# Kernel tuning notes

Measured on AMD Instinct MI355X. Metric: run time of the kernel, lower is better.

## Reference

```python
import jax, jax.numpy as jnp
import numpy as np

N, D, E, K, CAP = 16384, 1024, 64, 2, 640

def setup_inputs() -> dict:
    key = jax.random.key(0)
    k1, k2, k3 = jax.random.split(key, 3)
    x = jax.random.normal(k1, (N, D), dtype=jnp.float32)
    Wr = jax.random.normal(k2, (D, E), dtype=jnp.float32) / np.sqrt(D)
    br = jnp.zeros((E,), dtype=jnp.float32)
    We = jax.random.normal(k3, (E, D, D), dtype=jnp.float32) / np.sqrt(D)
    return {"x": x, "Wr": Wr, "br": br, "We": We, "k": K, "capacity": CAP}

def _route(x, Wr, br, k, num_experts):
    logits = x @ Wr + br                                  # [N, E]
    top_k_vals, top_k_idxs = jax.lax.top_k(logits, k)     # [N, k]
    gates = jax.nn.softmax(top_k_vals, axis=-1)           # [N, k]
    # flatten k-major like the original: transpose((1,0)).flatten()
    flat = top_k_idxs.T.reshape(-1)                       # [k*N]
    expert_mask = (flat[:, None] == jnp.arange(num_experts)).astype(jnp.int32)
    buffer_idxs = jnp.cumsum(expert_mask, axis=0) * expert_mask - 1  # [k*N, E]
    buffer_idxs = buffer_idxs.reshape(k, -1, num_experts)            # [k, N, E]
    dispatch_idxs = buffer_idxs.transpose(2, 0, 1).max(axis=1)       # [E, N]
    combine_idxs = buffer_idxs.max(axis=-1).T                        # [N, k]
    return gates, top_k_idxs, dispatch_idxs, combine_idxs

def reference(x, Wr, br, We, k, capacity):
    num_experts = Wr.shape[1]
    gates, top_k_idxs, dispatch_idxs, combine_idxs = _route(x, Wr, br, k, num_experts)
    # dispatch: scatter tokens into per-expert capacity buffers; unassigned (-1)
    # and overflow (>= capacity) tokens land in the dropped slot `capacity`.
    d_idx = jnp.where((dispatch_idxs < 0) | (dispatch_idxs > capacity), capacity, dispatch_idxs)
    def scatter_one(idx):
        return jnp.zeros((capacity + 1, x.shape[-1]), x.dtype).at[idx].set(x)[:-1]
    dispatched = jax.vmap(scatter_one)(d_idx)             # [E, C, D]
    # per-expert linear (the wrap()/vmap-ed expert), grouped GEMM
    expert_out = jax.nn.relu(jnp.einsum('ecd,edh->ech', dispatched, We))
    # combine: gather back, pad row `capacity` yields zeros for dropped tokens
    padded = jnp.pad(expert_out, ((0, 0), (0, 1), (0, 0)))
    c_idx = jnp.where((combine_idxs < 0) | (combine_idxs > capacity), capacity, combine_idxs)
    combined = padded[top_k_idxs, c_idx]                  # [N, k, D]
    return jnp.einsum('nk,nkd->nd', gates, combined)      # [N, D]
```

## Files before the change

### kernel.cpp

```cpp
#include <hip/hip_runtime.h>
#include <hip/hip_bf16.h>
#include <cstdint>
#include <cstddef>

#define N_TOK 16384
#define DIM   1024
#define NEXP  64
#define CAPACITY 640

typedef __bf16 bf16x8 __attribute__((ext_vector_type(8)));
typedef float  f32x4  __attribute__((ext_vector_type(4)));

__device__ __forceinline__ unsigned short f2bf(float f) {
    union { float f; unsigned int u; } a; a.f = f;
    unsigned int r = a.u + 0x7FFFu + ((a.u >> 16) & 1u);
    return (unsigned short)(r >> 16);
}

__global__ __launch_bounds__(256) void router_convert(
    const float* __restrict__ x, const float* __restrict__ Wr,
    const float* __restrict__ br, const float* __restrict__ We,
    unsigned short* __restrict__ xb, unsigned short* __restrict__ WeB,
    int* __restrict__ top2i, float* __restrict__ gates2,
    int* __restrict__ hist, float* __restrict__ out)
{
    __shared__ __align__(16) float smem[2][64][68];
    const int tid = threadIdx.x;

    if (blockIdx.x >= 8448) {
        const int z = blockIdx.x - 8448;
        float4* o = (float4*)(out + (size_t)z * 32768);
        const float4 zero = make_float4(0.f, 0.f, 0.f, 0.f);
#pragma unroll
        for (int l = 0; l < 32; l++) o[l * 256 + tid] = zero;
        return;
    }

    if (blockIdx.x >= 256) {
        const int b   = blockIdx.x - 256;
        const int e   = b >> 7;
        const int nt  = (b >> 4) & 7;
        const int ksi = b & 15;
        unsigned short (*T)[132] = (unsigned short (*)[132])smem;
        const int tc  = (tid & 31) * 4;
        const int tr  = tid >> 5;
        const float* src = We + ((size_t)e << 20) + (size_t)(ksi * 64) * DIM + nt * 128;
#pragma unroll
        for (int l = 0; l < 8; l++) {
            int dr = l * 8 + tr;
            float4 v = *(const float4*)(src + (size_t)dr * DIM + tc);
            ushort4 u = make_ushort4(f2bf(v.x), f2bf(v.y), f2bf(v.z), f2bf(v.w));
            *(ushort4*)&T[dr][tc] = u;
        }
        __syncthreads();
        unsigned short* dst = WeB + ((size_t)b << 13);
#pragma unroll
        for (int i = 0; i < 4; i++) {
            int p = i * 256 + tid;
            int kq = p >> 7, col = p & 127;
            unsigned int w0 = (unsigned int)T[kq * 8 + 0][col] | ((unsigned int)T[kq * 8 + 1][col] << 16);
            unsigned int w1 = (unsigned int)T[kq * 8 + 2][col] | ((unsigned int)T[kq * 8 + 3][col] << 16);
            unsigned int w2 = (unsigned int)T[kq * 8 + 4][col] | ((unsigned int)T[kq * 8 + 5][col] << 16);
            unsigned int w3 = (unsigned int)T[kq * 8 + 6][col] | ((unsigned int)T[kq * 8 + 7][col] << 16);
            *(uint4*)(dst + (size_t)p * 8) = make_uint4(w0, w1, w2, w3);
        }
        return;
    }

    float (*xs)[68] = smem[0];
    float (*wT)[68] = smem[1];
    const int t0  = blockIdx.x * 64;
    const int tm  = tid >> 4;
    const int te  = tid & 15;

    float acc[4][4];
#pragma unroll
    for (int i = 0; i < 4; i++)
#pragma unroll
        for (int j = 0; j < 4; j++) acc[i][j] = 0.f;

    for (int ks = 0; ks < DIM; ks += 64) {
        __syncthreads();
#pragma unroll
        for (int l = 0; l < 4; l++) {
            int row = l * 16 + tm;
            int col = te * 4;
            float4 v = *(const float4*)(x + (size_t)(t0 + row) * DIM + ks + col);
            *(float4*)&xs[row][col] = v;
            ushort4 b = make_ushort4(f2bf(v.x), f2bf(v.y), f2bf(v.z), f2bf(v.w));
            *(ushort4*)(xb + (size_t)(t0 + row) * DIM + ks + col) = b;
        }
#pragma unroll
        for (int l = 0; l < 4; l++) {
            int kr = l * 16 + tm;
            int ec = te * 4;
            float4 v = *(const float4*)(Wr + (size_t)(ks + kr) * NEXP + ec);
            wT[ec + 0][kr] = v.x; wT[ec + 1][kr] = v.y;
            wT[ec + 2][kr] = v.z; wT[ec + 3][kr] = v.w;
        }
        __syncthreads();
#pragma unroll 4
        for (int kk = 0; kk < 64; kk += 4) {
            float4 xv[4], wv[4];
#pragma unroll
            for (int i = 0; i < 4; i++) xv[i] = *(float4*)&xs[tm + i * 16][kk];
#pragma unroll
            for (int j = 0; j < 4; j++) wv[j] = *(float4*)&wT[te + j * 16][kk];
#pragma unroll
            for (int i = 0; i < 4; i++)
#pragma unroll
                for (int j = 0; j < 4; j++)
                    acc[i][j] += xv[i].x * wv[j].x + xv[i].y * wv[j].y +
                                 xv[i].z * wv[j].z + xv[i].w * wv[j].w;
        }
    }
    __syncthreads();
#pragma unroll
    for (int i = 0; i < 4; i++)
#pragma unroll
        for (int j = 0; j < 4; j++)
            xs[tm + i * 16][te + j * 16] = acc[i][j] + br[te + j * 16];
    __syncthreads();
    if (tid < 64) {
        int n = t0 + tid;
        float v1 = -1e30f, v2 = -1e30f; int i1 = 0, i2 = 0;
        for (int e = 0; e < 64; e++) {
            float v = xs[tid][e];
            if (v > v1)      { v2 = v1; i2 = i1; v1 = v; i1 = e; }
            else if (v > v2) { v2 = v;  i2 = e; }
        }
        float g0 = 1.f / (1.f + expf(v2 - v1));
        top2i[n * 2 + 0] = i1; top2i[n * 2 + 1] = i2;
        gates2[n * 2 + 0] = g0; gates2[n * 2 + 1] = 1.f - g0;
        atomicAdd(&hist[(n >> 8) * NEXP + i1], 1);
        atomicAdd(&hist[(64 + (n >> 8)) * NEXP + i2], 1);
    }
}

__global__ __launch_bounds__(64) void rank_kernel(
    const int* __restrict__ top2i, const float* __restrict__ gates2,
    const int* __restrict__ hist, int* __restrict__ list_tok,
    float* __restrict__ list_gate, int* __restrict__ cntc)
{
    int lane = threadIdx.x;
    int c = blockIdx.x;
    int cnt_reg = 0;
#pragma unroll 4
    for (int cc = 0; cc < c; cc++) cnt_reg += hist[cc * NEXP + lane];
    unsigned long long below = (1ull << lane) - 1ull;
    for (int r = 0; r < 4; r++) {
        int p = c * 256 + r * 64 + lane;
        int k = p >> 14, n = p & 16383;
        int e = top2i[n * 2 + k];
        int slot = 0;
#pragma unroll 1
        for (int q = 0; q < NEXP; q++) {
            unsigned long long mask = __ballot(e == q);
            int base = __shfl(cnt_reg, q);
            if (e == q) slot = base + __popcll(mask & below);
            if (lane == q) cnt_reg += (int)__popcll(mask);
        }
        if (slot < CAPACITY) {
            list_tok[e * CAPACITY + slot]  = n;
            list_gate[e * CAPACITY + slot] = gates2[n * 2 + k];
        }
    }
    if (c == 127) cntc[lane] = cnt_reg < CAPACITY ? cnt_reg : CAPACITY;
}

__global__ __launch_bounds__(256) void moe_gemm3(
    const unsigned short* __restrict__ xb, const unsigned short* __restrict__ WeB,
    const int* __restrict__ list_tok, const float* __restrict__ list_gate,
    const int* __restrict__ cntc, float* __restrict__ out)
{
    const int bid = blockIdx.x;
    const int e   = bid / 40;
    const int rem = bid % 40;
    const int mt  = rem >> 3;
    const int nt  = rem & 7;
    const int cnt = cntc[e];
    if (mt * 128 >= cnt) return;
    int valid = cnt - mt * 128; if (valid > 128) valid = 128;

    __shared__ __align__(16) unsigned short As[2][8192];
    __shared__ __align__(16) unsigned short Bs[2][8192];
    __shared__ int   tok_s[128];
    __shared__ float gate_s[128];

    const int tid = threadIdx.x;
    if (tid < 128) {
        int slot = mt * 128 + tid;
        bool v = tid < valid;
        tok_s[tid]  = v ? list_tok[e * CAPACITY + slot]  : list_tok[e * CAPACITY];
        gate_s[tid] = v ? list_gate[e * CAPACITY + slot] : 0.f;
    }
    __syncthreads();

    const int arow  = tid & 127;
    const int ahalf = tid >> 7;
    const unsigned short* aG = xb + (size_t)tok_s[arow] * DIM + ahalf * 8;
    const unsigned short* bG = WeB + ((size_t)(e * 8 + nt) * 16) * 8192 + (size_t)tid * 8;

    const int wv   = tid >> 6;
    const int lane = tid & 63;
    const int wm = wv >> 1, wn = wv & 1;
    const int fm = lane & 15, kq = lane >> 4;

    f32x4 acc[4][4];
#pragma unroll
    for (int i = 0; i < 4; i++)
#pragma unroll
        for (int j = 0; j < 4; j++) acc[i][j] = (f32x4){0.f, 0.f, 0.f, 0.f};

    auto stage = [&](int buf, int ksi) {
#pragma unroll
        for (int i = 0; i < 4; i++) {
            const int ldsOff = (i * 256 + wv * 64) * 8;
            __builtin_amdgcn_global_load_lds(
                (const __attribute__((address_space(1))) unsigned int*)(aG + ksi * 64 + i * 16),
                (__attribute__((address_space(3))) unsigned int*)(&As[buf][ldsOff]), 16, 0, 0);
            __builtin_amdgcn_global_load_lds(
                (const __attribute__((address_space(1))) unsigned int*)(bG + (size_t)ksi * 8192 + i * 2048),
                (__attribute__((address_space(3))) unsigned int*)(&Bs[buf][ldsOff]), 16, 0, 0);
        }
    };
    auto compute = [&](int buf) {
#pragma unroll
        for (int kk = 0; kk < 2; kk++) {
            union { uint4 u; bf16x8 v; } fa[4], fb[4];
#pragma unroll
            for (int i = 0; i < 4; i++)
                fa[i].u = *(const uint4*)(&As[buf][((kk * 4 + kq) * 128 + wm * 64 + i * 16 + fm) * 8]);
#pragma unroll
            for (int j = 0; j < 4; j++)
                fb[j].u = *(const uint4*)(&Bs[buf][((kk * 4 + kq) * 128 + wn * 64 + j * 16 + fm) * 8]);
#pragma unroll
            for (int i = 0; i < 4; i++)
#pragma unroll
                for (int j = 0; j < 4; j++)
                    acc[i][j] = __builtin_amdgcn_mfma_f32_16x16x32_bf16(
                        fa[i].v, fb[j].v, acc[i][j], 0, 0, 0);
        }
    };

    stage(0, 0);
    __syncthreads();
    int cur = 0;
#pragma unroll 1
    for (int ksi = 1; ksi < 16; ksi++) {
        stage(cur ^ 1, ksi);
        compute(cur);
        __syncthreads();
        cur ^= 1;
    }
    compute(cur);

    const int col0 = nt * 128 + wn * 64 + fm;
#pragma unroll
    for (int i = 0; i < 4; i++) {
        int rbase = wm * 64 + i * 16 + kq * 4;
#pragma unroll
        for (int j = 0; j < 4; j++) {
            int col = col0 + j * 16;
#pragma unroll
            for (int r = 0; r < 4; r++) {
                int row = rbase + r;
                if (row < valid) {
                    float v = acc[i][j][r];
                    v = fmaxf(v, 0.f) * gate_s[row];
                    atomicAdd(out + (size_t)tok_s[row] * DIM + col, v);
                }
            }
        }
    }
}

#define MT 128
#define NT 128
#define BK 32
#define LDA 36

__global__ __launch_bounds__(256) void moe_gemm(
    const unsigned short* __restrict__ xb, const float* __restrict__ We,
    const int* __restrict__ list_tok, const float* __restrict__ list_gate,
    const int* __restrict__ cntc, float* __restrict__ out)
{
    const int bid = blockIdx.x;
    const int e   = bid / 40;
    const int rem = bid % 40;
    const int mt  = rem >> 3;
    const int nt  = rem & 7;
    const int cnt = cntc[e];
    if (mt * MT >= cnt) return;
    int valid = cnt - mt * MT; if (valid > MT) valid = MT;

    __shared__ unsigned short As[MT * LDA];
    __shared__ unsigned short Bs[NT * LDA];
    __shared__ int   tok_s[MT];
    __shared__ float gate_s[MT];

    const int tid = threadIdx.x;
    if (tid < MT) {
        int slot = mt * MT + tid;
        bool v = tid < valid;
        tok_s[tid]  = v ? list_tok[e * CAPACITY + slot]  : list_tok[e * CAPACITY];
        gate_s[tid] = v ? list_gate[e * CAPACITY + slot] : 0.f;
    }
    __syncthreads();

    const int arow = tid >> 1, ah = tid & 1;
    const unsigned short* aptr = xb + (size_t)tok_s[arow] * DIM + ah * 16;
    const int bn0 = (tid & 31) * 4;
    const int bkr = (tid >> 5) * 4;
    const float* bptr = We + (size_t)e * DIM * DIM + (size_t)bkr * DIM + nt * NT + bn0;

    f32x4 acc[4][4];
#pragma unroll
    for (int i = 0; i < 4; i++)
#pragma unroll
        for (int j = 0; j < 4; j++) acc[i][j] = (f32x4){0.f, 0.f, 0.f, 0.f};

    const int lane = tid & 63, wave = tid >> 6;
    const int wm = wave >> 1, wn = wave & 1;
    const int fm = lane & 15, kq = lane >> 4;

    for (int ks = 0; ks < DIM; ks += BK) {
        __syncthreads();
        uint4 a0 = *(const uint4*)(aptr + ks);
        uint4 a1 = *(const uint4*)(aptr + ks + 8);
        {
            unsigned short* d = &As[arow * LDA + ah * 16];
            *(uint2*)(d + 0)  = make_uint2(a0.x, a0.y);
            *(uint2*)(d + 4)  = make_uint2(a0.z, a0.w);
            *(uint2*)(d + 8)  = make_uint2(a1.x, a1.y);
            *(uint2*)(d + 12) = make_uint2(a1.z, a1.w);
        }
        {
            float4 b[4];
#pragma unroll
            for (int j = 0; j < 4; j++)
                b[j] = *(const float4*)(bptr + (size_t)(ks + j) * DIM);
            union { float4 v; float f[4]; } u0, u1, u2, u3;
            u0.v = b[0]; u1.v = b[1]; u2.v = b[2]; u3.v = b[3];
#pragma unroll
            for (int cc = 0; cc < 4; cc++) {
                unsigned int lo = (unsigned int)f2bf(u0.f[cc]) | ((unsigned int)f2bf(u1.f[cc]) << 16);
                unsigned int hi = (unsigned int)f2bf(u2.f[cc]) | ((unsigned int)f2bf(u3.f[cc]) << 16);
                *(uint2*)&Bs[(bn0 + cc) * LDA + bkr] = make_uint2(lo, hi);
            }
        }
        __syncthreads();
        union { uint2 u[2]; bf16x8 v; } fa[4], fb[4];
#pragma unroll
        for (int i = 0; i < 4; i++) {
            const unsigned short* s = &As[(wm * 64 + i * 16 + fm) * LDA + kq * 8];
            fa[i].u[0] = *(const uint2*)(s);
            fa[i].u[1] = *(const uint2*)(s + 4);
        }
#pragma unroll
        for (int j = 0; j < 4; j++) {
            const unsigned short* s = &Bs[(wn * 64 + j * 16 + fm) * LDA + kq * 8];
            fb[j].u[0] = *(const uint2*)(s);
            fb[j].u[1] = *(const uint2*)(s + 4);
        }
#pragma unroll
        for (int i = 0; i < 4; i++)
#pragma unroll
            for (int j = 0; j < 4; j++)
                acc[i][j] = __builtin_amdgcn_mfma_f32_16x16x32_bf16(
                    fa[i].v, fb[j].v, acc[i][j], 0, 0, 0);
    }

    const int col0 = nt * NT + wn * 64 + fm;
#pragma unroll
    for (int i = 0; i < 4; i++) {
        int rbase = wm * 64 + i * 16 + kq * 4;
#pragma unroll
        for (int j = 0; j < 4; j++) {
            int col = col0 + j * 16;
#pragma unroll
            for (int r = 0; r < 4; r++) {
                int row = rbase + r;
                if (row < valid) {
                    float v = acc[i][j][r];
                    v = fmaxf(v, 0.f) * gate_s[row];
                    atomicAdd(out + (size_t)tok_s[row] * DIM + col, v);
                }
            }
        }
    }
}

extern "C" void kernel_launch(void* const* d_in, const int* in_sizes, int n_in,
                              void* d_out, int out_size, void* d_ws, size_t ws_size,
                              hipStream_t stream)
{
    const float* x  = (const float*)d_in[0];
    const float* Wr = (const float*)d_in[1];
    const float* br = (const float*)d_in[2];
    const float* We = (const float*)d_in[3];
    float* out = (float*)d_out;

    char* ws = (char*)d_ws;
    size_t off = 0;
    unsigned short* xb = (unsigned short*)(ws + off); off += (size_t)N_TOK * DIM * 2;
    int*   top2i     = (int*)(ws + off);   off += (size_t)N_TOK * 2 * 4;
    float* gates2    = (float*)(ws + off); off += (size_t)N_TOK * 2 * 4;
    int*   hist      = (int*)(ws + off);   off += 128 * NEXP * 4;
    int*   cntc      = (int*)(ws + off);   off += NEXP * 4;
    int*   list_tok  = (int*)(ws + off);   off += NEXP * CAPACITY * 4;
    float* list_gate = (float*)(ws + off); off += NEXP * CAPACITY * 4;
    off = (off + 255) & ~(size_t)255;
    unsigned short* WeB = (unsigned short*)(ws + off);
    size_t need = off + (size_t)NEXP * DIM * DIM * 2;

    const bool fast = ws_size >= need;

    hipMemsetAsync(hist, 0, 128 * NEXP * 4, stream);
    if (fast) {
        router_convert<<<8960, 256, 0, stream>>>(x, Wr, br, We, xb, WeB,
                                                 top2i, gates2, hist, out);
        rank_kernel<<<128, 64, 0, stream>>>(top2i, gates2, hist,
                                            list_tok, list_gate, cntc);
        moe_gemm3<<<NEXP * 40, 256, 0, stream>>>(xb, WeB, list_tok, list_gate,
                                                 cntc, out);
    } else {
        hipMemsetAsync(out, 0, (size_t)N_TOK * DIM * 4, stream);
        router_convert<<<256, 256, 0, stream>>>(x, Wr, br, We, xb, xb,
                                                top2i, gates2, hist, out);
        rank_kernel<<<128, 64, 0, stream>>>(top2i, gates2, hist,
                                            list_tok, list_gate, cntc);
        moe_gemm<<<NEXP * 40, 256, 0, stream>>>(xb, We, list_tok, list_gate,
                                                cntc, out);
    }
}
```

Before: 680.3 us.

## Replace atomic scatter-add with per-slot stores and a separate combine kernel

The expert GEMM now writes each gated result to a dedicated row indexed by (k, token) with plain stores instead of atomicAdd into the output. A new combine kernel sums the two top-k rows per token and writes the output, so the output no longer needs zeroing and the router launch shrinks accordingly. This removes atomic contention and the zero-fill pass but adds a large intermediate buffer and an extra read/write pass over it. The path is used only when the workspace is big enough.

```diff
diff --git a/kernel.cpp b/kernel.cpp
--- a/kernel.cpp
+++ b/kernel.cpp
@@ -140,7 +140,8 @@
 __global__ __launch_bounds__(64) void rank_kernel(
     const int* __restrict__ top2i, const float* __restrict__ gates2,
     const int* __restrict__ hist, int* __restrict__ list_tok,
-    float* __restrict__ list_gate, int* __restrict__ cntc)
+    float* __restrict__ list_gate, int* __restrict__ cntc,
+    int* __restrict__ slot_of)
 {
     int lane = threadIdx.x;
     int c = blockIdx.x;
@@ -160,18 +161,20 @@
             if (e == q) slot = base + __popcll(mask & below);
             if (lane == q) cnt_reg += (int)__popcll(mask);
         }
+        slot_of[p] = slot;
         if (slot < CAPACITY) {
-            list_tok[e * CAPACITY + slot]  = n;
+            list_tok[e * CAPACITY + slot]  = n | (k << 16);
             list_gate[e * CAPACITY + slot] = gates2[n * 2 + k];
         }
     }
     if (c == 127) cntc[lane] = cnt_reg < CAPACITY ? cnt_reg : CAPACITY;
 }
 
-__global__ __launch_bounds__(256) void moe_gemm3(
+template <int MODE>
+__global__ __launch_bounds__(256) void moe_gemm3t(
     const unsigned short* __restrict__ xb, const unsigned short* __restrict__ WeB,
     const int* __restrict__ list_tok, const float* __restrict__ list_gate,
-    const int* __restrict__ cntc, float* __restrict__ out)
+    const int* __restrict__ cntc, float* __restrict__ outc)
 {
     const int bid = blockIdx.x;
     const int e   = bid / 40;
@@ -185,13 +188,17 @@
     __shared__ __align__(16) unsigned short As[2][8192];
     __shared__ __align__(16) unsigned short Bs[2][8192];
     __shared__ int   tok_s[128];
+    __shared__ int   crow_s[128];
     __shared__ float gate_s[128];
 
     const int tid = threadIdx.x;
     if (tid < 128) {
         int slot = mt * 128 + tid;
         bool v = tid < valid;
-        tok_s[tid]  = v ? list_tok[e * CAPACITY + slot]  : list_tok[e * CAPACITY];
+        int raw = v ? list_tok[e * CAPACITY + slot] : list_tok[e * CAPACITY];
+        int n   = raw & 0x3FFF;
+        tok_s[tid]  = n;
+        crow_s[tid] = ((raw >> 16) << 14) | n;
         gate_s[tid] = v ? list_gate[e * CAPACITY + slot] : 0.f;
     }
     __syncthreads();
@@ -268,11 +275,34 @@
                 if (row < valid) {
                     float v = acc[i][j][r];
                     v = fmaxf(v, 0.f) * gate_s[row];
-                    atomicAdd(out + (size_t)tok_s[row] * DIM + col, v);
+                    if (MODE == 0)
+                        atomicAdd(outc + (size_t)tok_s[row] * DIM + col, v);
+                    else
+                        outc[(size_t)crow_s[row] * DIM + col] = v;
                 }
             }
         }
     }
+}
+
+__global__ __launch_bounds__(256) void combine_kernel(
+    const float* __restrict__ comb, const int* __restrict__ slot_of,
+    float* __restrict__ out)
+{
+    const int n = blockIdx.x;
+    const int d = threadIdx.x;
+    const int s0 = slot_of[n];
+    const int s1 = slot_of[N_TOK + n];
+    float4 r = make_float4(0.f, 0.f, 0.f, 0.f);
+    if (s0 < CAPACITY) {
+        float4 v = ((const float4*)(comb + (size_t)n * DIM))[d];
+        r.x = v.x; r.y = v.y; r.z = v.z; r.w = v.w;
+    }
+    if (s1 < CAPACITY) {
+        float4 v = ((const float4*)(comb + ((size_t)N_TOK + n) * DIM))[d];
+        r.x += v.x; r.y += v.y; r.z += v.z; r.w += v.w;
+    }
+    ((float4*)(out + (size_t)n * DIM))[d] = r;
 }
 
 #define MT 128
@@ -303,7 +333,8 @@
     if (tid < MT) {
         int slot = mt * MT + tid;
         bool v = tid < valid;
-        tok_s[tid]  = v ? list_tok[e * CAPACITY + slot]  : list_tok[e * CAPACITY];
+        int raw = v ? list_tok[e * CAPACITY + slot] : list_tok[e * CAPACITY];
+        tok_s[tid]  = raw & 0x3FFF;
         gate_s[tid] = v ? list_gate[e * CAPACITY + slot] : 0.f;
     }
     __syncthreads();
@@ -410,26 +441,39 @@
     int*   cntc      = (int*)(ws + off);   off += NEXP * 4;
     int*   list_tok  = (int*)(ws + off);   off += NEXP * CAPACITY * 4;
     float* list_gate = (float*)(ws + off); off += NEXP * CAPACITY * 4;
+    int*   slot_of   = (int*)(ws + off);   off += (size_t)N_TOK * 2 * 4;
     off = (off + 255) & ~(size_t)255;
     unsigned short* WeB = (unsigned short*)(ws + off);
     size_t need = off + (size_t)NEXP * DIM * DIM * 2;
-
-    const bool fast = ws_size >= need;
+    size_t off2 = (need + 255) & ~(size_t)255;
+    float* comb = (float*)(ws + off2);
+    size_t need2 = off2 + (size_t)N_TOK * 2 * DIM * 4;
+
+    const bool fast2 = ws_size >= need2;
+    const bool fast  = ws_size >= need;
 
     hipMemsetAsync(hist, 0, 128 * NEXP * 4, stream);
-    if (fast) {
+    if (fast2) {
+        router_convert<<<8448, 256, 0, stream>>>(x, Wr, br, We, xb, WeB,
+                                                 top2i, gates2, hist, out);
+        rank_kernel<<<128, 64, 0, stream>>>(top2i, gates2, hist,
+                                            list_tok, list_gate, cntc, slot_of);
+        moe_gemm3t<1><<<NEXP * 40, 256, 0, stream>>>(xb, WeB, list_tok,
+                                                     list_gate, cntc, comb);
+        combine_kernel<<<N_TOK, 256, 0, stream>>>(comb, slot_of, out);
+    } else if (fast) {
         router_convert<<<8960, 256, 0, stream>>>(x, Wr, br, We, xb, WeB,
                                                  top2i, gates2, hist, out);
         rank_kernel<<<128, 64, 0, stream>>>(top2i, gates2, hist,
-                                            list_tok, list_gate, cntc);
-        moe_gemm3<<<NEXP * 40, 256, 0, stream>>>(xb, WeB, list_tok, list_gate,
-                                                 cntc, out);
+                                            list_tok, list_gate, cntc, slot_of);
+        moe_gemm3t<0><<<NEXP * 40, 256, 0, stream>>>(xb, WeB, list_tok,
+                                                     list_gate, cntc, out);
     } else {
         hipMemsetAsync(out, 0, (size_t)N_TOK * DIM * 4, stream);
         router_convert<<<256, 256, 0, stream>>>(x, Wr, br, We, xb, xb,
                                                 top2i, gates2, hist, out);
         rank_kernel<<<128, 64, 0, stream>>>(top2i, gates2, hist,
-                                            list_tok, list_gate, cntc);
+                                            list_tok, list_gate, cntc, slot_of);
         moe_gemm<<<NEXP * 40, 256, 0, stream>>>(xb, We, list_tok, list_gate,
                                                 cntc, out);
     }
```

After: 678.1 us. No clear change (-0.3%).
